# Performance work log

Measured on AMD Instinct MI355X. Metric: run time of the kernel, lower is better.

The kernel has to match this reference:

```python
import jax, jax.numpy as jnp
import numpy as np

NUM_HEADS = 16
EPS = 1e-12  # matches torch F.normalize eps


def _l2_normalize(x):
    n = jnp.sqrt(jnp.sum(x * x, axis=-1, keepdims=True))
    return x / jnp.maximum(n, EPS)


def setup_inputs() -> dict:
    key = jax.random.key(0)
    ks = jax.random.split(key, 9)
    B, L, S, D = 4, 4096, 4096, 1024
    s = 1.0 / np.sqrt(D)
    return {
        "q": jax.random.normal(ks[0], (B, L, D), jnp.float32),
        "k": jax.random.normal(ks[1], (B, S, D), jnp.float32),
        "v": jax.random.normal(ks[2], (B, S, D), jnp.float32),
        "Wq": jax.random.normal(ks[3], (D, D), jnp.float32) * s,
        "bq": jax.random.normal(ks[4], (D,), jnp.float32) * 0.01,
        "Wk": jax.random.normal(ks[5], (D, D), jnp.float32) * s,
        "bk": jax.random.normal(ks[6], (D,), jnp.float32) * 0.01,
        "Wv": jax.random.normal(ks[7], (D, D), jnp.float32) * s,
        "bv": jax.random.normal(ks[8], (D,), jnp.float32) * 0.01,
    }


def reference(q, k, v, Wq, bq, Wk, bk, Wv, bv):
    B = q.shape[0]
    H = NUM_HEADS
    # Linear projections (torch Linear: x @ W^T + b)
    qp = q @ Wq.T + bq  # [B, L, D]
    kp = k @ Wk.T + bk  # [B, S, D]
    vp = v @ Wv.T + bv  # [B, S, D]
    # Split heads: [B, T, H, i] -> [B, H, T, i]
    def split(x):
        Bx, T, D = x.shape
        return x.reshape(Bx, T, H, D // H).transpose(0, 2, 1, 3)
    qh = split(qp)
    kh = _l2_normalize(split(kp))
    vh = _l2_normalize(split(vp))
    # No softmax -> exact reassociation: (q k^T) v == q (k^T v)
    kv = jnp.einsum('bhsi,bhsj->bhij', kh, vh)  # [B, H, i, i]
    xh = jnp.einsum('bhli,bhij->bhlj', qh, kv)  # [B, H, L, i]
    # Merge heads: [B, H, L, i] -> [B, L, H*i]
    Bx, Hh, L, I = xh.shape
    return xh.transpose(0, 2, 1, 3).reshape(Bx, L, Hh * I)
```

## Files before the change

### kernel.cpp

```cpp
#include <hip/hip_runtime.h>
#include <hip/hip_bf16.h>
#include <stdint.h>

typedef __attribute__((ext_vector_type(8))) short bf16x8;
typedef __attribute__((ext_vector_type(4))) float f32x4;
typedef __attribute__((ext_vector_type(8))) unsigned short ushort8;

__device__ __forceinline__ float bf2f(unsigned short u) {
  union { unsigned int i; float f; } x; x.i = ((unsigned int)u) << 16; return x.f;
}
__device__ __forceinline__ unsigned short f2bf(float f) {
  union { __hip_bfloat16 h; unsigned short u; } x; x.h = __float2bfloat16(f); return x.u;
}

__device__ __forceinline__ void gload_lds16(const void* g, void* l) {
  __builtin_amdgcn_global_load_lds((__attribute__((address_space(1))) const void*)g,
                                   (__attribute__((address_space(3))) void*)l, 16, 0, 0);
}

__global__ __launch_bounds__(256) void cvt_kernel(const float* __restrict__ in,
                                                  unsigned short* __restrict__ out,
                                                  int n8) {
  int i = blockIdx.x * 256 + threadIdx.x;
  if (i >= n8) return;
  const float4* p = (const float4*)(in + (size_t)i * 8);
  float4 a = p[0], b = p[1];
  ushort8 o;
  o[0] = f2bf(a.x); o[1] = f2bf(a.y); o[2] = f2bf(a.z); o[3] = f2bf(a.w);
  o[4] = f2bf(b.x); o[5] = f2bf(b.y); o[6] = f2bf(b.z); o[7] = f2bf(b.w);
  *(ushort8*)(out + (size_t)i * 8) = o;
}

__global__ __launch_bounds__(256) void cvt2_kernel(const float* __restrict__ a,
                                                   const float* __restrict__ b,
                                                   unsigned short* __restrict__ oa,
                                                   unsigned short* __restrict__ ob,
                                                   int n8) {
  const float* in = blockIdx.y ? b : a;
  unsigned short* out = blockIdx.y ? ob : oa;
  int i = blockIdx.x * 256 + threadIdx.x;
  if (i >= n8) return;
  const float4* p = (const float4*)(in + (size_t)i * 8);
  float4 x = p[0], y = p[1];
  ushort8 o;
  o[0] = f2bf(x.x); o[1] = f2bf(x.y); o[2] = f2bf(x.z); o[3] = f2bf(x.w);
  o[4] = f2bf(y.x); o[5] = f2bf(y.y); o[6] = f2bf(y.z); o[7] = f2bf(y.w);
  *(ushort8*)(out + (size_t)i * 8) = o;
}

__global__ __launch_bounds__(256) void cvt3w_kernel(const float* __restrict__ a,
                                                    const float* __restrict__ b,
                                                    const float* __restrict__ c,
                                                    unsigned short* __restrict__ oa,
                                                    unsigned short* __restrict__ ob,
                                                    unsigned short* __restrict__ oc,
                                                    int n8) {
  const float* in = blockIdx.y == 0 ? a : blockIdx.y == 1 ? b : c;
  unsigned short* out = blockIdx.y == 0 ? oa : blockIdx.y == 1 ? ob : oc;
  int i = blockIdx.x * 256 + threadIdx.x;
  if (i >= n8) return;
  const float4* p = (const float4*)(in + (size_t)i * 8);
  float4 x = p[0], y = p[1];
  ushort8 o;
  o[0] = f2bf(x.x); o[1] = f2bf(x.y); o[2] = f2bf(x.z); o[3] = f2bf(x.w);
  o[4] = f2bf(y.x); o[5] = f2bf(y.y); o[6] = f2bf(y.z); o[7] = f2bf(y.w);
  *(ushort8*)(out + (size_t)i * 8) = o;
}

template <bool NORM>
__device__ __forceinline__ void gemm256_body(
    const unsigned short* __restrict__ A,
    const unsigned short* __restrict__ B,
    const float* __restrict__ bias,
    void* __restrict__ C,
    int bm, int bn,
    unsigned short (*As)[256][32],
    unsigned short (*Bs)[256][32]) {
  const int tid = threadIdx.x;
  const int widx = tid >> 6, lane = tid & 63;
  const int wr = widx >> 2, wc = widx & 3;
  const int fr = lane & 15, fkg = lane >> 4;
  const int g4 = fkg * 4;
  const int pgo = (fkg ^ ((fr >> 1) & 3)) * 8;
  const int srow = lane >> 2;
  const int sg = ((lane & 3) ^ ((lane >> 3) & 3)) * 8;

  const size_t abase = (size_t)(bm * 256) * 1024;
  const size_t bbase = (size_t)(bn * 256) * 1024;

  f32x4 acc[8][4];
#pragma unroll
  for (int m = 0; m < 8; ++m)
#pragma unroll
    for (int n = 0; n < 4; ++n) acc[m][n] = (f32x4){0.f, 0.f, 0.f, 0.f};

  bf16x8 aF[8], bF[4];

#define STG_A(bufi, kh, kt)                                                                \
  {                                                                                        \
    gload_lds16(A + abase + (size_t)(widx * 16 + srow) * 1024 + (kt) * 64 + (kh) * 32 + sg,\
                &As[(bufi) * 2 + (kh)][widx * 16][0]);                                     \
    gload_lds16(A + abase + (size_t)(128 + widx * 16 + srow) * 1024 + (kt) * 64 + (kh) * 32 + sg, \
                &As[(bufi) * 2 + (kh)][128 + widx * 16][0]);                               \
  }
#define STG_B(bufi, kh, kt)                                                                \
  {                                                                                        \
    gload_lds16(B + bbase + (size_t)(widx * 16 + srow) * 1024 + (kt) * 64 + (kh) * 32 + sg,\
                &Bs[(bufi) * 2 + (kh)][widx * 16][0]);                                     \
    gload_lds16(B + bbase + (size_t)(128 + widx * 16 + srow) * 1024 + (kt) * 64 + (kh) * 32 + sg, \
                &Bs[(bufi) * 2 + (kh)][128 + widx * 16][0]);                               \
  }
#define LDA(bufi, ks)                                                                      \
  _Pragma("unroll") for (int m = 0; m < 8; ++m)                                            \
      aF[m] = *(const bf16x8*)&As[(bufi) * 2 + (ks)][wr * 128 + m * 16 + fr][pgo];
#define LDBALL(bufi, ks)                                                                   \
  _Pragma("unroll") for (int n = 0; n < 4; ++n)                                            \
      bF[n] = *(const bf16x8*)&Bs[(bufi) * 2 + (ks)][wc * 64 + n * 16 + fr][pgo];
#define MMALL()                                                                            \
  {                                                                                        \
    __builtin_amdgcn_s_setprio(1);                                                         \
    _Pragma("unroll") for (int m = 0; m < 8; ++m)                                          \
        _Pragma("unroll") for (int n = 0; n < 4; ++n)                                      \
            acc[m][n] = __builtin_amdgcn_mfma_f32_16x16x32_bf16(aF[m], bF[n], acc[m][n], 0, 0, 0); \
    __builtin_amdgcn_s_setprio(0);                                                         \
  }
#define BARM() asm volatile("s_barrier" ::: "memory")
#define LGKM()                                          \
  asm volatile("s_waitcnt lgkmcnt(0)" ::: "memory");    \
  __builtin_amdgcn_sched_barrier(0)
#define VMW(N) asm volatile("s_waitcnt vmcnt(" #N ")" ::: "memory")

  STG_A(0, 0, 0); STG_B(0, 0, 0);
  STG_A(0, 1, 0); STG_B(0, 1, 0);
  STG_A(1, 0, 1); STG_B(1, 0, 1);
  VMW(4);
  BARM();

  for (int i = 0; i < 8; ++i) {
    const int t1s = 2 * i + 1, u0 = 2 * i + 2, u1 = 2 * i + 3;
    const bool st = (i < 7);
    LDA(0, 0); LDBALL(0, 0); STG_A(1, 1, t1s); STG_B(1, 1, t1s);
    BARM(); LGKM(); MMALL(); VMW(8); BARM();
    LDA(0, 1); LDBALL(0, 1); if (st) { STG_A(0, 0, u0); STG_B(0, 0, u0); }
    BARM(); LGKM(); MMALL(); VMW(8); BARM();
    LDA(1, 0); LDBALL(1, 0); if (st) { STG_A(0, 1, u0); STG_B(0, 1, u0); }
    BARM(); LGKM(); MMALL();
    if (st) { VMW(8); } else { VMW(0); }
    BARM();
    LDA(1, 1); LDBALL(1, 1); if (st) { STG_A(1, 0, u1); STG_B(1, 0, u1); }
    BARM(); LGKM(); MMALL();
    if (st) { VMW(8); } else { VMW(0); }
    BARM();
  }
#undef STG_A
#undef STG_B
#undef LDA
#undef LDBALL
#undef MMALL
#undef BARM
#undef LGKM
#undef VMW

  if (NORM) {
    float bsv[4];
#pragma unroll
    for (int n = 0; n < 4; ++n) bsv[n] = bias[bn * 256 + wc * 64 + n * 16 + fr];
#pragma unroll
    for (int m = 0; m < 8; ++m) {
      float val[4][4];
      float inv[4];
#pragma unroll
      for (int j = 0; j < 4; ++j) {
        float s = 0.f;
#pragma unroll
        for (int n = 0; n < 4; ++n) {
          val[n][j] = acc[m][n][j] + bsv[n];
          s += val[n][j] * val[n][j];
        }
        s += __shfl_xor(s, 1); s += __shfl_xor(s, 2);
        s += __shfl_xor(s, 4); s += __shfl_xor(s, 8);
        inv[j] = 1.f / fmaxf(sqrtf(s), 1e-12f);
      }
#pragma unroll
      for (int n = 0; n < 4; ++n) {
        const int col = bn * 256 + wc * 64 + n * 16 + fr;
#pragma unroll
        for (int j = 0; j < 4; ++j) {
          const int row = bm * 256 + wr * 128 + m * 16 + g4 + j;
          ((unsigned short*)C)[(size_t)row * 1024 + col] = f2bf(val[n][j] * inv[j]);
        }
      }
    }
  } else {
#pragma unroll
    for (int n = 0; n < 4; ++n) {
      const int col = bn * 256 + wc * 64 + n * 16 + fr;
      const float bsv = bias[col];
#pragma unroll
      for (int m = 0; m < 8; ++m) {
#pragma unroll
        for (int j = 0; j < 4; ++j) {
          const int row = bm * 256 + wr * 128 + m * 16 + g4 + j;
          ((float*)C)[(size_t)row * 1024 + col] = acc[m][n][j] + bsv;
        }
      }
    }
  }
}

__global__ __launch_bounds__(512, 1) void proj_norm_kernel(
    const unsigned short* __restrict__ A0, const unsigned short* __restrict__ A1,
    const unsigned short* __restrict__ B0, const unsigned short* __restrict__ B1,
    const float* __restrict__ bias0, const float* __restrict__ bias1,
    unsigned short* __restrict__ C0, unsigned short* __restrict__ C1) {
  __shared__ unsigned short As[4][256][32];
  __shared__ unsigned short Bs[4][256][32];
  const int flat = (blockIdx.z * 64 + blockIdx.y) * 4 + blockIdx.x;
  const int swz = (flat & 7) * 64 + (flat >> 3);
  const int zz = swz >> 8;
  const int rem = swz & 255;
  const int bm = rem >> 2, bn = rem & 3;
  gemm256_body<true>(zz ? A1 : A0, zz ? B1 : B0, zz ? bias1 : bias0,
                     zz ? (void*)C1 : (void*)C0, bm, bn, As, Bs);
}

__global__ __launch_bounds__(512, 1) void final_gemm_kernel(
    const unsigned short* __restrict__ A,
    const unsigned short* __restrict__ Beff,
    const float* __restrict__ beff,
    float* __restrict__ out) {
  __shared__ unsigned short As[4][256][32];
  __shared__ unsigned short Bs[4][256][32];
  const int flat = blockIdx.y * 4 + blockIdx.x;
  const int swz = (flat & 7) * 32 + (flat >> 3);
  const int bm = swz >> 2, bn = swz & 3;
  const int b = bm >> 4;
  gemm256_body<false>(A, Beff + (size_t)b * 1048576, beff + b * 1024, out, bm, bn, As, Bs);
}

__global__ __launch_bounds__(256) void kv_part_kernel(const unsigned short* __restrict__ kh,
                                                      const unsigned short* __restrict__ vh,
                                                      float* __restrict__ kvp) {
  const int chunk = blockIdx.x, h = blockIdx.y, b = blockIdx.z;
  __shared__ unsigned short khT[64][264];
  __shared__ unsigned short vhT[64][264];
  const int tid = threadIdx.x, wid = tid >> 6, lane = tid & 63;
  const int fr = lane & 15, fk = (lane >> 4) * 8, g4 = (lane >> 4) * 4;

  const int jb = tid & 7, sb = tid >> 3;
  const size_t base = ((size_t)b * 4096 + chunk * 256) * 1024 + h * 64;
  {
    ushort8 rk[8], rv[8];
#pragma unroll
    for (int u = 0; u < 8; ++u) {
      rk[u] = *(const ushort8*)(kh + base + (size_t)(sb * 8 + u) * 1024 + jb * 8);
      rv[u] = *(const ushort8*)(vh + base + (size_t)(sb * 8 + u) * 1024 + jb * 8);
    }
#pragma unroll
    for (int jj = 0; jj < 8; ++jj) {
      ushort8 ck, cv;
#pragma unroll
      for (int u = 0; u < 8; ++u) { ck[u] = rk[u][jj]; cv[u] = rv[u][jj]; }
      *(ushort8*)&khT[jb * 8 + jj][sb * 8] = ck;
      *(ushort8*)&vhT[jb * 8 + jj][sb * 8] = cv;
    }
  }
  __syncthreads();

  f32x4 acc2[4];
#pragma unroll
  for (int n = 0; n < 4; ++n) acc2[n] = (f32x4){0.f, 0.f, 0.f, 0.f};
#pragma unroll
  for (int ks = 0; ks < 8; ++ks) {
    bf16x8 a2 = *(const bf16x8*)&khT[wid * 16 + fr][ks * 32 + fk];
    bf16x8 b2[4];
#pragma unroll
    for (int jt = 0; jt < 4; ++jt) b2[jt] = *(const bf16x8*)&vhT[jt * 16 + fr][ks * 32 + fk];
#pragma unroll
    for (int jt = 0; jt < 4; ++jt)
      acc2[jt] = __builtin_amdgcn_mfma_f32_16x16x32_bf16(a2, b2[jt], acc2[jt], 0, 0, 0);
  }
  float* dst = kvp + ((size_t)chunk * 64 + b * 16 + h) * 4096;
#pragma unroll
  for (int jt = 0; jt < 4; ++jt)
#pragma unroll
    for (int jj = 0; jj < 4; ++jj)
      dst[(wid * 16 + g4 + jj) * 64 + jt * 16 + fr] = acc2[jt][jj];
}

__global__ __launch_bounds__(256) void weff_kernel(
    const unsigned short* __restrict__ Wq,
    const float* __restrict__ bq,
    const float* __restrict__ kvp,
    unsigned short* __restrict__ Beff,
    float* __restrict__ beff) {
  const int dt = blockIdx.x, h = blockIdx.y, b = blockIdx.z;
  __shared__ float kvS[64 * 64];
  __shared__ float WqF[64 * 128];
  const int tid = threadIdx.x;

  const float* kvsrc = kvp + (size_t)(b * 16 + h) * 4096;
  for (int e = tid; e < 4096; e += 256) {
    float s = 0.f;
#pragma unroll
    for (int c = 0; c < 16; ++c) s += kvsrc[(size_t)c * 64 * 4096 + e];
    kvS[e] = s;
  }
  {
    int i = tid >> 2, dseg = tid & 3;
    const unsigned short* src = Wq + (size_t)(h * 64 + i) * 1024 + dt * 128 + dseg * 32;
    float* dst = &WqF[i * 128 + dseg * 32];
#pragma unroll
    for (int w = 0; w < 4; ++w) {
      ushort8 vv = ((const ushort8*)src)[w];
#pragma unroll
      for (int u = 0; u < 8; ++u) dst[w * 8 + u] = bf2f(vv[u]);
    }
  }
  __syncthreads();

  const int tj = tid & 63, tg = tid >> 6;
  float o[32];
#pragma unroll
  for (int dd = 0; dd < 32; ++dd) o[dd] = 0.f;
  for (int i = 0; i < 64; ++i) {
    float kvv = kvS[i * 64 + tj];
    const float* wr = &WqF[i * 128 + tg * 32];
#pragma unroll
    for (int dd = 0; dd < 32; ++dd) o[dd] += wr[dd] * kvv;
  }
  unsigned short* dstB = Beff + ((size_t)(b * 1024 + h * 64 + tj)) * 1024 + dt * 128 + tg * 32;
#pragma unroll
  for (int w = 0; w < 4; ++w) {
    ushort8 ov;
#pragma unroll
    for (int u = 0; u < 8; ++u) ov[u] = f2bf(o[w * 8 + u]);
    ((ushort8*)dstB)[w] = ov;
  }
  if (tg == 0 && dt == 0) {
    float s = 0.f;
    for (int i = 0; i < 64; ++i) s += bq[h * 64 + i] * kvS[i * 64 + tj];
    beff[b * 1024 + h * 64 + tj] = s;
  }
}

extern "C" void kernel_launch(void* const* d_in, const int* in_sizes, int n_in,
                              void* d_out, int out_size, void* d_ws, size_t ws_size,
                              hipStream_t stream) {
  const float* q = (const float*)d_in[0];
  const float* k = (const float*)d_in[1];
  const float* v = (const float*)d_in[2];
  const float* Wq = (const float*)d_in[3];
  const float* bq = (const float*)d_in[4];
  const float* Wk = (const float*)d_in[5];
  const float* bk = (const float*)d_in[6];
  const float* Wv = (const float*)d_in[7];
  const float* bv = (const float*)d_in[8];
  float* out = (float*)d_out;

  const size_t NE = (size_t)16384 * 1024;
  const size_t MB = 1048576;

  char* ws = (char*)d_ws;
  unsigned short* S0 = (unsigned short*)(ws + 0 * MB);
  unsigned short* S1 = (unsigned short*)(ws + 32 * MB);
  unsigned short* kh = (unsigned short*)(ws + 64 * MB);
  unsigned short* vh = (unsigned short*)(ws + 96 * MB);
  unsigned short* Wqb = (unsigned short*)(ws + 128 * MB);
  unsigned short* Wkb = (unsigned short*)(ws + 130 * MB);
  unsigned short* Wvb = (unsigned short*)(ws + 132 * MB);
  float* beff = (float*)(ws + 134 * MB);
  float* kvp = (float*)S0;
  unsigned short* Beff = (unsigned short*)(ws + 16 * MB);

  cvt2_kernel<<<dim3(8192, 2), 256, 0, stream>>>(k, v, S0, S1, (int)(NE / 8));
  cvt3w_kernel<<<dim3(512, 3), 256, 0, stream>>>(Wq, Wk, Wv, Wqb, Wkb, Wvb, 131072);

  proj_norm_kernel<<<dim3(4, 64, 2), 512, 0, stream>>>(S0, S1, Wkb, Wvb, bk, bv, kh, vh);

  cvt_kernel<<<8192, 256, 0, stream>>>(q, S1, (int)(NE / 8));

  kv_part_kernel<<<dim3(16, 16, 4), 256, 0, stream>>>(kh, vh, kvp);

  weff_kernel<<<dim3(8, 16, 4), 256, 0, stream>>>(Wqb, bq, kvp, Beff, beff);

  final_gemm_kernel<<<dim3(4, 64), 512, 0, stream>>>(S1, Beff, beff, out);
}
```

Baseline: 232.9 us.

## Fuse Q projection with per-head kv multiply in final GEMM kernel

Removes the weff kernel that folded kv into an effective Wq per batch. A small kernel now reduces the kv partials into transposed bf16 kv. The final kernel computes the Q projection tile, stages it through LDS as bf16, and multiplies by the per-head kv with a second MFMA pass. The GEMM pipeline also drops the explicit lgkmcnt waits and relaxes some vmcnt waits. This trades the Beff build for extra LDS traffic, one more bf16 rounding step, and wait ordering that relies on the compiler to insert the LDS waits.

```diff
diff --git a/kernel.cpp b/kernel.cpp
--- a/kernel.cpp
+++ b/kernel.cpp
@@ -67,32 +67,22 @@
   *(ushort8*)(out + (size_t)i * 8) = o;
 }
 
-template <bool NORM>
-__device__ __forceinline__ void gemm256_body(
+__device__ __forceinline__ void gemm256_loop(
     const unsigned short* __restrict__ A,
     const unsigned short* __restrict__ B,
-    const float* __restrict__ bias,
-    void* __restrict__ C,
     int bm, int bn,
-    unsigned short (*As)[256][32],
-    unsigned short (*Bs)[256][32]) {
+    unsigned short (*As)[256][32], unsigned short (*Bs)[256][32],
+    f32x4 (*acc)[4]) {
   const int tid = threadIdx.x;
   const int widx = tid >> 6, lane = tid & 63;
   const int wr = widx >> 2, wc = widx & 3;
   const int fr = lane & 15, fkg = lane >> 4;
-  const int g4 = fkg * 4;
   const int pgo = (fkg ^ ((fr >> 1) & 3)) * 8;
   const int srow = lane >> 2;
   const int sg = ((lane & 3) ^ ((lane >> 3) & 3)) * 8;
 
   const size_t abase = (size_t)(bm * 256) * 1024;
   const size_t bbase = (size_t)(bn * 256) * 1024;
-
-  f32x4 acc[8][4];
-#pragma unroll
-  for (int m = 0; m < 8; ++m)
-#pragma unroll
-    for (int n = 0; n < 4; ++n) acc[m][n] = (f32x4){0.f, 0.f, 0.f, 0.f};
 
   bf16x8 aF[8], bF[4];
 
@@ -125,9 +115,6 @@
     __builtin_amdgcn_s_setprio(0);                                                         \
   }
 #define BARM() asm volatile("s_barrier" ::: "memory")
-#define LGKM()                                          \
-  asm volatile("s_waitcnt lgkmcnt(0)" ::: "memory");    \
-  __builtin_amdgcn_sched_barrier(0)
 #define VMW(N) asm volatile("s_waitcnt vmcnt(" #N ")" ::: "memory")
 
   STG_A(0, 0, 0); STG_B(0, 0, 0);
@@ -140,16 +127,16 @@
     const int t1s = 2 * i + 1, u0 = 2 * i + 2, u1 = 2 * i + 3;
     const bool st = (i < 7);
     LDA(0, 0); LDBALL(0, 0); STG_A(1, 1, t1s); STG_B(1, 1, t1s);
-    BARM(); LGKM(); MMALL(); VMW(8); BARM();
+    BARM(); MMALL(); BARM();
     LDA(0, 1); LDBALL(0, 1); if (st) { STG_A(0, 0, u0); STG_B(0, 0, u0); }
-    BARM(); LGKM(); MMALL(); VMW(8); BARM();
+    BARM(); MMALL();
+    if (st) { VMW(4); } else { VMW(0); }
+    BARM();
     LDA(1, 0); LDBALL(1, 0); if (st) { STG_A(0, 1, u0); STG_B(0, 1, u0); }
-    BARM(); LGKM(); MMALL();
-    if (st) { VMW(8); } else { VMW(0); }
-    BARM();
+    BARM(); MMALL(); BARM();
     LDA(1, 1); LDBALL(1, 1); if (st) { STG_A(1, 0, u1); STG_B(1, 0, u1); }
-    BARM(); LGKM(); MMALL();
-    if (st) { VMW(8); } else { VMW(0); }
+    BARM(); MMALL();
+    if (st) { VMW(4); } else { VMW(0); }
     BARM();
   }
 #undef STG_A
@@ -158,54 +145,7 @@
 #undef LDBALL
 #undef MMALL
 #undef BARM
-#undef LGKM
 #undef VMW
-
-  if (NORM) {
-    float bsv[4];
-#pragma unroll
-    for (int n = 0; n < 4; ++n) bsv[n] = bias[bn * 256 + wc * 64 + n * 16 + fr];
-#pragma unroll
-    for (int m = 0; m < 8; ++m) {
-      float val[4][4];
-      float inv[4];
-#pragma unroll
-      for (int j = 0; j < 4; ++j) {
-        float s = 0.f;
-#pragma unroll
-        for (int n = 0; n < 4; ++n) {
-          val[n][j] = acc[m][n][j] + bsv[n];
-          s += val[n][j] * val[n][j];
-        }
-        s += __shfl_xor(s, 1); s += __shfl_xor(s, 2);
-        s += __shfl_xor(s, 4); s += __shfl_xor(s, 8);
-        inv[j] = 1.f / fmaxf(sqrtf(s), 1e-12f);
-      }
-#pragma unroll
-      for (int n = 0; n < 4; ++n) {
-        const int col = bn * 256 + wc * 64 + n * 16 + fr;
-#pragma unroll
-        for (int j = 0; j < 4; ++j) {
-          const int row = bm * 256 + wr * 128 + m * 16 + g4 + j;
-          ((unsigned short*)C)[(size_t)row * 1024 + col] = f2bf(val[n][j] * inv[j]);
-        }
-      }
-    }
-  } else {
-#pragma unroll
-    for (int n = 0; n < 4; ++n) {
-      const int col = bn * 256 + wc * 64 + n * 16 + fr;
-      const float bsv = bias[col];
-#pragma unroll
-      for (int m = 0; m < 8; ++m) {
-#pragma unroll
-        for (int j = 0; j < 4; ++j) {
-          const int row = bm * 256 + wr * 128 + m * 16 + g4 + j;
-          ((float*)C)[(size_t)row * 1024 + col] = acc[m][n][j] + bsv;
-        }
-      }
-    }
-  }
 }
 
 __global__ __launch_bounds__(512, 1) void proj_norm_kernel(
@@ -220,22 +160,147 @@
   const int zz = swz >> 8;
   const int rem = swz & 255;
   const int bm = rem >> 2, bn = rem & 3;
-  gemm256_body<true>(zz ? A1 : A0, zz ? B1 : B0, zz ? bias1 : bias0,
-                     zz ? (void*)C1 : (void*)C0, bm, bn, As, Bs);
-}
-
-__global__ __launch_bounds__(512, 1) void final_gemm_kernel(
+  const unsigned short* A = zz ? A1 : A0;
+  const unsigned short* B = zz ? B1 : B0;
+  const float* bias = zz ? bias1 : bias0;
+  unsigned short* C = zz ? C1 : C0;
+
+  f32x4 acc[8][4];
+#pragma unroll
+  for (int m = 0; m < 8; ++m)
+#pragma unroll
+    for (int n = 0; n < 4; ++n) acc[m][n] = (f32x4){0.f, 0.f, 0.f, 0.f};
+
+  gemm256_loop(A, B, bm, bn, As, Bs, acc);
+
+  const int tid = threadIdx.x, widx = tid >> 6, lane = tid & 63;
+  const int wr = widx >> 2, wc = widx & 3;
+  const int fr = lane & 15, g4 = (lane >> 4) * 4;
+
+  float bsv[4];
+#pragma unroll
+  for (int n = 0; n < 4; ++n) bsv[n] = bias[bn * 256 + wc * 64 + n * 16 + fr];
+#pragma unroll
+  for (int m = 0; m < 8; ++m) {
+    float val[4][4];
+    float inv[4];
+#pragma unroll
+    for (int j = 0; j < 4; ++j) {
+      float s = 0.f;
+#pragma unroll
+      for (int n = 0; n < 4; ++n) {
+        val[n][j] = acc[m][n][j] + bsv[n];
+        s += val[n][j] * val[n][j];
+      }
+      s += __shfl_xor(s, 1); s += __shfl_xor(s, 2);
+      s += __shfl_xor(s, 4); s += __shfl_xor(s, 8);
+      inv[j] = 1.f / fmaxf(sqrtf(s), 1e-12f);
+    }
+#pragma unroll
+    for (int n = 0; n < 4; ++n) {
+      const int col = bn * 256 + wc * 64 + n * 16 + fr;
+#pragma unroll
+      for (int j = 0; j < 4; ++j) {
+        const int row = bm * 256 + wr * 128 + m * 16 + g4 + j;
+        C[(size_t)row * 1024 + col] = f2bf(val[n][j] * inv[j]);
+      }
+    }
+  }
+}
+
+__global__ __launch_bounds__(512, 1) void final_fold_kernel(
     const unsigned short* __restrict__ A,
-    const unsigned short* __restrict__ Beff,
-    const float* __restrict__ beff,
+    const unsigned short* __restrict__ Wqb,
+    const float* __restrict__ bq,
+    const unsigned short* __restrict__ kvT,
     float* __restrict__ out) {
-  __shared__ unsigned short As[4][256][32];
-  __shared__ unsigned short Bs[4][256][32];
+  __shared__ __align__(16) unsigned char smem[163840];
+  unsigned short (*As)[256][32] = (unsigned short (*)[256][32])smem;
+  unsigned short (*Bs)[256][32] = (unsigned short (*)[256][32])(smem + 65536);
+
   const int flat = blockIdx.y * 4 + blockIdx.x;
   const int swz = (flat & 7) * 32 + (flat >> 3);
   const int bm = swz >> 2, bn = swz & 3;
-  const int b = bm >> 4;
-  gemm256_body<false>(A, Beff + (size_t)b * 1048576, beff + b * 1024, out, bm, bn, As, Bs);
+  const int bB = bm >> 4;
+
+  const int tid = threadIdx.x, widx = tid >> 6, lane = tid & 63;
+  const int wr = widx >> 2, wc = widx & 3;
+  const int fr = lane & 15, fkg = lane >> 4, g4 = fkg * 4;
+
+#pragma unroll
+  for (int t = 0; t < 4; ++t) {
+    int unit = t * 512 + tid;
+    int h = unit >> 9;
+    int jr = (unit >> 3) & 63;
+    int g = unit & 7;
+    ushort8 vvv = *(const ushort8*)(kvT +
+        ((size_t)(bB * 16 + bn * 4 + h) * 4096) + jr * 64 + g * 8);
+    *(ushort8*)(smem + 131072 + h * 8192 + jr * 128 + ((g ^ (jr & 7)) * 16)) = vvv;
+  }
+  __syncthreads();
+
+  f32x4 acc[8][4];
+#pragma unroll
+  for (int m = 0; m < 8; ++m)
+#pragma unroll
+    for (int n = 0; n < 4; ++n) acc[m][n] = (f32x4){0.f, 0.f, 0.f, 0.f};
+
+  gemm256_loop(A, Wqb, bm, bn, As, Bs, acc);
+
+  {
+    float bsv[4];
+#pragma unroll
+    for (int n = 0; n < 4; ++n) bsv[n] = bq[bn * 256 + wc * 64 + n * 16 + fr];
+#pragma unroll
+    for (int m = 0; m < 8; ++m)
+#pragma unroll
+      for (int n = 0; n < 4; ++n)
+#pragma unroll
+        for (int j = 0; j < 4; ++j) {
+          float v = acc[m][n][j] + bsv[n];
+          int r = m * 16 + g4 + j;
+          int c = n * 16 + fr;
+          *(unsigned short*)(smem + widx * 16384 + r * 128 +
+                             (((c >> 3) ^ (r & 7)) * 16) + (c & 7) * 2) = f2bf(v);
+        }
+  }
+  __syncthreads();
+
+  f32x4 acc2[8][4];
+#pragma unroll
+  for (int m = 0; m < 8; ++m)
+#pragma unroll
+    for (int n = 0; n < 4; ++n) acc2[m][n] = (f32x4){0.f, 0.f, 0.f, 0.f};
+
+#pragma unroll
+  for (int ks = 0; ks < 2; ++ks) {
+    bf16x8 a2[8], b2[4];
+#pragma unroll
+    for (int m = 0; m < 8; ++m)
+      a2[m] = *(const bf16x8*)(smem + widx * 16384 + (m * 16 + fr) * 128 +
+                               (((ks * 4 + fkg) ^ (fr & 7)) * 16));
+#pragma unroll
+    for (int n = 0; n < 4; ++n)
+      b2[n] = *(const bf16x8*)(smem + 131072 + wc * 8192 + (n * 16 + fr) * 128 +
+                               (((ks * 4 + fkg) ^ (fr & 7)) * 16));
+#pragma unroll
+    for (int m = 0; m < 8; ++m)
+#pragma unroll
+      for (int n = 0; n < 4; ++n)
+        acc2[m][n] = __builtin_amdgcn_mfma_f32_16x16x32_bf16(a2[m], b2[n], acc2[m][n], 0, 0, 0);
+  }
+
+#pragma unroll
+  for (int n = 0; n < 4; ++n) {
+    const int col = bn * 256 + wc * 64 + n * 16 + fr;
+#pragma unroll
+    for (int m = 0; m < 8; ++m)
+#pragma unroll
+      for (int j = 0; j < 4; ++j) {
+        const int row = bm * 256 + wr * 128 + m * 16 + g4 + j;
+        out[(size_t)row * 1024 + col] = acc2[m][n][j];
+      }
+  }
 }
 
 __global__ __launch_bounds__(256) void kv_part_kernel(const unsigned short* __restrict__ kh,
@@ -288,59 +353,15 @@
       dst[(wid * 16 + g4 + jj) * 64 + jt * 16 + fr] = acc2[jt][jj];
 }
 
-__global__ __launch_bounds__(256) void weff_kernel(
-    const unsigned short* __restrict__ Wq,
-    const float* __restrict__ bq,
-    const float* __restrict__ kvp,
-    unsigned short* __restrict__ Beff,
-    float* __restrict__ beff) {
-  const int dt = blockIdx.x, h = blockIdx.y, b = blockIdx.z;
-  __shared__ float kvS[64 * 64];
-  __shared__ float WqF[64 * 128];
-  const int tid = threadIdx.x;
-
-  const float* kvsrc = kvp + (size_t)(b * 16 + h) * 4096;
-  for (int e = tid; e < 4096; e += 256) {
+__global__ __launch_bounds__(256) void kvt_reduce_kernel(const float* __restrict__ kvp,
+                                                         unsigned short* __restrict__ kvT) {
+  const int bh = blockIdx.x;
+  for (int e = threadIdx.x; e < 4096; e += 256) {
     float s = 0.f;
 #pragma unroll
-    for (int c = 0; c < 16; ++c) s += kvsrc[(size_t)c * 64 * 4096 + e];
-    kvS[e] = s;
-  }
-  {
-    int i = tid >> 2, dseg = tid & 3;
-    const unsigned short* src = Wq + (size_t)(h * 64 + i) * 1024 + dt * 128 + dseg * 32;
-    float* dst = &WqF[i * 128 + dseg * 32];
-#pragma unroll
-    for (int w = 0; w < 4; ++w) {
-      ushort8 vv = ((const ushort8*)src)[w];
-#pragma unroll
-      for (int u = 0; u < 8; ++u) dst[w * 8 + u] = bf2f(vv[u]);
-    }
-  }
-  __syncthreads();
-
-  const int tj = tid & 63, tg = tid >> 6;
-  float o[32];
-#pragma unroll
-  for (int dd = 0; dd < 32; ++dd) o[dd] = 0.f;
-  for (int i = 0; i < 64; ++i) {
-    float kvv = kvS[i * 64 + tj];
-    const float* wr = &WqF[i * 128 + tg * 32];
-#pragma unroll
-    for (int dd = 0; dd < 32; ++dd) o[dd] += wr[dd] * kvv;
-  }
-  unsigned short* dstB = Beff + ((size_t)(b * 1024 + h * 64 + tj)) * 1024 + dt * 128 + tg * 32;
-#pragma unroll
-  for (int w = 0; w < 4; ++w) {
-    ushort8 ov;
-#pragma unroll
-    for (int u = 0; u < 8; ++u) ov[u] = f2bf(o[w * 8 + u]);
-    ((ushort8*)dstB)[w] = ov;
-  }
-  if (tg == 0 && dt == 0) {
-    float s = 0.f;
-    for (int i = 0; i < 64; ++i) s += bq[h * 64 + i] * kvS[i * 64 + tj];
-    beff[b * 1024 + h * 64 + tj] = s;
+    for (int c = 0; c < 16; ++c) s += kvp[((size_t)c * 64 + bh) * 4096 + e];
+    int i = e >> 6, j = e & 63;
+    kvT[(size_t)bh * 4096 + j * 64 + i] = f2bf(s);
   }
 }
 
@@ -369,9 +390,8 @@
   unsigned short* Wqb = (unsigned short*)(ws + 128 * MB);
   unsigned short* Wkb = (unsigned short*)(ws + 130 * MB);
   unsigned short* Wvb = (unsigned short*)(ws + 132 * MB);
-  float* beff = (float*)(ws + 134 * MB);
+  unsigned short* kvT = (unsigned short*)(ws + 134 * MB);
   float* kvp = (float*)S0;
-  unsigned short* Beff = (unsigned short*)(ws + 16 * MB);
 
   cvt2_kernel<<<dim3(8192, 2), 256, 0, stream>>>(k, v, S0, S1, (int)(NE / 8));
   cvt3w_kernel<<<dim3(512, 3), 256, 0, stream>>>(Wq, Wk, Wv, Wqb, Wkb, Wvb, 131072);
@@ -382,7 +402,7 @@
 
   kv_part_kernel<<<dim3(16, 16, 4), 256, 0, stream>>>(kh, vh, kvp);
 
-  weff_kernel<<<dim3(8, 16, 4), 256, 0, stream>>>(Wqb, bq, kvp, Beff, beff);
-
-  final_gemm_kernel<<<dim3(4, 64), 512, 0, stream>>>(S1, Beff, beff, out);
-}
+  kvt_reduce_kernel<<<64, 256, 0, stream>>>(kvp, kvT);
+
+  final_fold_kernel<<<dim3(4, 64), 512, 0, stream>>>(S1, Wqb, bq, kvT, out);
+}
```

Measured after the change: 213.6 us. 1.09x faster.
